# Performance work log

Hardware: AMD Instinct MI355X
Metric: run time of the kernel (lower is better)

Reference implementation:

```python
import jax, jax.numpy as jnp
import numpy as np

B = 32768
C = 1000


def setup_inputs() -> dict:
    key = jax.random.key(0)
    k1, k2, k3 = jax.random.split(key, 3)
    output = jax.random.normal(k1, (B, C), dtype=jnp.float32)
    target = jax.random.randint(k2, (B,), 0, C, dtype=jnp.int64)
    # loss_lams rows are (approx) probability vectors from the previous epoch
    lams = jax.random.uniform(k3, (C, C), dtype=jnp.float32)
    loss_lams = lams / jnp.sum(lams, axis=1, keepdims=True)
    return {"output": output, "target": target, "loss_lams": loss_lams}


def reference(output, target, loss_lams):
    """OLS loss forward.

    Returns (loss, cur_epoch_lams_update, cur_epoch_cnt_update) where the
    updates are the increments added to the zero-initialized per-epoch state
    (update_loss_lams side effect), and loss = 0.5*CE + 0.5*softCE.
    """
    b, c = output.shape
    target = target.astype(jnp.int32)

    # --- update_loss_lams: softmax, keep samples where argmax == target,
    # scatter-add their prob vectors into the row of their target class ---
    probs = jax.nn.softmax(output, axis=1)                      # [B, C]
    pred = jnp.argmax(probs, axis=1)                            # [B]
    correct = (pred == target).astype(output.dtype)             # [B]
    lams_update = jax.ops.segment_sum(probs * correct[:, None], target,
                                      num_segments=c)           # [C, C]
    cnt_update = jax.ops.segment_sum(correct, target, num_segments=c)  # [C]

    # --- loss: 0.5 * hard CE + 0.5 * soft CE with loss_lams soft labels ---
    log_probs = jax.nn.log_softmax(output, axis=1)              # [B, C]
    ce = -jnp.mean(jnp.take_along_axis(log_probs, target[:, None], axis=1))
    soft_targets = loss_lams[target]                            # [B, C] gather
    soft_ce = -jnp.sum(log_probs * soft_targets) / b
    loss = 0.5 * ce + 0.5 * soft_ce
    return loss, lams_update, cnt_update
```

## Files before the change

### kernel.cpp

```cpp
#include <hip/hip_runtime.h>
#include <math.h>

constexpr int B_ROWS = 32768;
constexpr int C_COLS = 1000;
constexpr int VEC4   = C_COLS / 4;

using f4 = __attribute__((ext_vector_type(4))) float;

__global__ __launch_bounds__(256, 8) void ols_main(
    const float* __restrict__ output,
    const int*   __restrict__ target,
    const float* __restrict__ lams,
    float*       __restrict__ partials,
    float*       __restrict__ lams_upd,
    float*       __restrict__ cnt_upd)
{
    __shared__ float s_max[4];
    __shared__ float s_red[4][3];
    __shared__ float s_xt;

    const int tid  = threadIdx.x;
    const int lane = tid & 63;
    const int wid  = tid >> 6;
    const int row  = blockIdx.x;
    const bool act = tid < VEC4;

    const int t = target[row];

    f4 x = act ? reinterpret_cast<const f4*>(output + (size_t)row * C_COLS)[tid]
               : (f4){-INFINITY, -INFINITY, -INFINITY, -INFINITY};
    f4 l = act ? reinterpret_cast<const f4*>(lams + (size_t)t * C_COLS)[tid]
               : (f4){0.0f, 0.0f, 0.0f, 0.0f};

    float m = fmaxf(fmaxf(x[0], x[1]), fmaxf(x[2], x[3]));
#pragma unroll
    for (int off = 32; off > 0; off >>= 1) m = fmaxf(m, __shfl_xor(m, off));
    if (lane == 0) s_max[wid] = m;

    const int q = t >> 2, e = t & 3;
    if (tid == q)
        s_xt = (e == 0) ? x[0] : (e == 1) ? x[1] : (e == 2) ? x[2] : x[3];
    __syncthreads();

    m = fmaxf(fmaxf(s_max[0], s_max[1]), fmaxf(s_max[2], s_max[3]));
    const float x_t = s_xt;

    float p0 = __expf(x[0] - m), p1 = __expf(x[1] - m);
    float p2 = __expf(x[2] - m), p3 = __expf(x[3] - m);
    float s   = (p0 + p1) + (p2 + p3);
    float dot = act ? (l[0]*x[0] + l[1]*x[1]) + (l[2]*x[2] + l[3]*x[3]) : 0.0f;
    float rs  = (l[0] + l[1]) + (l[2] + l[3]);
#pragma unroll
    for (int off = 32; off > 0; off >>= 1) {
        s   += __shfl_xor(s,   off);
        dot += __shfl_xor(dot, off);
        rs  += __shfl_xor(rs,  off);
    }
    if (lane == 0) { s_red[wid][0] = s; s_red[wid][1] = dot; s_red[wid][2] = rs; }
    __syncthreads();

    s = (s_red[0][0] + s_red[1][0]) + (s_red[2][0] + s_red[3][0]);

    if (tid == 0) {
        const float dT = (s_red[0][1] + s_red[1][1]) + (s_red[2][1] + s_red[3][1]);
        const float rT = (s_red[0][2] + s_red[1][2]) + (s_red[2][2] + s_red[3][2]);
        const float lse = m + __logf(s);
        partials[row] = 0.5f * ((lse - x_t) + (lse * rT - dT));
    }

    if (x_t == m) {
        const float inv = 1.0f / s;
        if (act) {
            float* dst = lams_upd + (size_t)t * C_COLS + 4 * tid;
            atomicAdd(dst + 0, p0 * inv);
            atomicAdd(dst + 1, p1 * inv);
            atomicAdd(dst + 2, p2 * inv);
            atomicAdd(dst + 3, p3 * inv);
        }
        if (tid == 0) atomicAdd(&cnt_upd[t], 1.0f);
    }
}

__global__ __launch_bounds__(256) void ols_reduce(
    const float* __restrict__ partials, float* __restrict__ d_loss)
{
    __shared__ float sm[4];
    const int lane = threadIdx.x & 63;
    const int wid  = threadIdx.x >> 6;
    const f4* p4 = reinterpret_cast<const f4*>(partials);
    float acc = 0.0f;
#pragma unroll
    for (int k = 0; k < 32; ++k) {
        f4 v = p4[threadIdx.x + k * 256];
        acc += (v[0] + v[1]) + (v[2] + v[3]);
    }
#pragma unroll
    for (int off = 32; off > 0; off >>= 1) acc += __shfl_xor(acc, off);
    if (lane == 0) sm[wid] = acc;
    __syncthreads();
    if (threadIdx.x == 0)
        *d_loss = ((sm[0] + sm[1]) + (sm[2] + sm[3])) * (1.0f / (float)B_ROWS);
}

extern "C" void kernel_launch(void* const* d_in, const int* in_sizes, int n_in,
                              void* d_out, int out_size, void* d_ws, size_t ws_size,
                              hipStream_t stream) {
    const float* output = (const float*)d_in[0];
    const int*   target = (const int*)d_in[1];
    const float* lams   = (const float*)d_in[2];

    float* out      = (float*)d_out;
    float* d_loss   = out;
    float* lams_upd = out + 1;
    float* cnt_upd  = out + 1 + C_COLS * C_COLS;
    float* partials = (float*)d_ws;

    hipMemsetAsync(d_out, 0, (size_t)out_size * sizeof(float), stream);

    ols_main<<<dim3(B_ROWS), dim3(256), 0, stream>>>(output, target, lams,
                                                     partials, lams_upd, cnt_upd);
    ols_reduce<<<dim3(1), dim3(256), 0, stream>>>(partials, d_loss);
}
```

Before: 202.2 us.

## Process multiple rows per block with register prefetch and single-barrier online softmax

Launches 2048 persistent-style blocks that each loop over 16 rows, prefetching the next row's logits and target into registers while the current row is processed. The block max is no longer a separate barrier step: each wave keeps its own max, and the per-wave sums are rescaled, which cuts the row's two syncthreads to one. Loss is accumulated per block, so the final reduce reads 2048 partials instead of 32768. The cost is a less parallel grid and extra exp calls, and the lams gather still waits on the target load with no prefetch.

After: 205.6 us. No clear change (+1.7%).

```diff
diff --git a/kernel.cpp b/kernel.cpp
--- a/kernel.cpp
+++ b/kernel.cpp
@@ -4,6 +4,8 @@
 constexpr int B_ROWS = 32768;
 constexpr int C_COLS = 1000;
 constexpr int VEC4   = C_COLS / 4;
+constexpr int NBLK   = 2048;
+constexpr int RPB    = B_ROWS / NBLK;
 
 using f4 = __attribute__((ext_vector_type(4))) float;
 
@@ -15,70 +17,98 @@
     float*       __restrict__ lams_upd,
     float*       __restrict__ cnt_upd)
 {
-    __shared__ float s_max[4];
-    __shared__ float s_red[4][3];
-    __shared__ float s_xt;
+    __shared__ float s_stat[2][4][4];
+    __shared__ float s_xt[2];
 
     const int tid  = threadIdx.x;
     const int lane = tid & 63;
     const int wid  = tid >> 6;
-    const int row  = blockIdx.x;
     const bool act = tid < VEC4;
 
-    const int t = target[row];
+    const f4 X_PAD = (f4){-INFINITY, -INFINITY, -INFINITY, -INFINITY};
 
-    f4 x = act ? reinterpret_cast<const f4*>(output + (size_t)row * C_COLS)[tid]
-               : (f4){-INFINITY, -INFINITY, -INFINITY, -INFINITY};
-    f4 l = act ? reinterpret_cast<const f4*>(lams + (size_t)t * C_COLS)[tid]
-               : (f4){0.0f, 0.0f, 0.0f, 0.0f};
+    float lossAcc = 0.0f;
 
-    float m = fmaxf(fmaxf(x[0], x[1]), fmaxf(x[2], x[3]));
+    int tb[2];
+    f4  xb[2];
+    tb[0] = target[blockIdx.x];
+    xb[0] = act ? reinterpret_cast<const f4*>(output + (size_t)blockIdx.x * C_COLS)[tid]
+                : X_PAD;
+
 #pragma unroll
-    for (int off = 32; off > 0; off >>= 1) m = fmaxf(m, __shfl_xor(m, off));
-    if (lane == 0) s_max[wid] = m;
+    for (int i = 0; i < RPB; ++i) {
+        const int cb = i & 1, nb = cb ^ 1;
 
-    const int q = t >> 2, e = t & 3;
-    if (tid == q)
-        s_xt = (e == 0) ? x[0] : (e == 1) ? x[1] : (e == 2) ? x[2] : x[3];
-    __syncthreads();
+        if (i + 1 < RPB) {
+            const int nrow = blockIdx.x + (i + 1) * NBLK;
+            tb[nb] = target[nrow];
+            xb[nb] = act ? reinterpret_cast<const f4*>(output + (size_t)nrow * C_COLS)[tid]
+                         : X_PAD;
+        }
 
-    m = fmaxf(fmaxf(s_max[0], s_max[1]), fmaxf(s_max[2], s_max[3]));
-    const float x_t = s_xt;
+        const int t = tb[cb];
+        const f4  x = xb[cb];
 
-    float p0 = __expf(x[0] - m), p1 = __expf(x[1] - m);
-    float p2 = __expf(x[2] - m), p3 = __expf(x[3] - m);
-    float s   = (p0 + p1) + (p2 + p3);
-    float dot = act ? (l[0]*x[0] + l[1]*x[1]) + (l[2]*x[2] + l[3]*x[3]) : 0.0f;
-    float rs  = (l[0] + l[1]) + (l[2] + l[3]);
+        const f4 l = act ? reinterpret_cast<const f4*>(lams + (size_t)t * C_COLS)[tid]
+                         : (f4){0.0f, 0.0f, 0.0f, 0.0f};
+
+        float mw = fmaxf(fmaxf(x[0], x[1]), fmaxf(x[2], x[3]));
 #pragma unroll
-    for (int off = 32; off > 0; off >>= 1) {
-        s   += __shfl_xor(s,   off);
-        dot += __shfl_xor(dot, off);
-        rs  += __shfl_xor(rs,  off);
-    }
-    if (lane == 0) { s_red[wid][0] = s; s_red[wid][1] = dot; s_red[wid][2] = rs; }
-    __syncthreads();
+        for (int off = 32; off > 0; off >>= 1) mw = fmaxf(mw, __shfl_xor(mw, off));
 
-    s = (s_red[0][0] + s_red[1][0]) + (s_red[2][0] + s_red[3][0]);
+        const float p0 = __expf(x[0] - mw), p1 = __expf(x[1] - mw);
+        const float p2 = __expf(x[2] - mw), p3 = __expf(x[3] - mw);
+        float s = (p0 + p1) + (p2 + p3);
+        float dot = act ? (l[0]*x[0] + l[1]*x[1]) + (l[2]*x[2] + l[3]*x[3]) : 0.0f;
+        float rs  = (l[0] + l[1]) + (l[2] + l[3]);
+#pragma unroll
+        for (int off = 32; off > 0; off >>= 1) {
+            s   += __shfl_xor(s,   off);
+            dot += __shfl_xor(dot, off);
+            rs  += __shfl_xor(rs,  off);
+        }
+        if (lane == 0) {
+            s_stat[cb][wid][0] = mw; s_stat[cb][wid][1] = s;
+            s_stat[cb][wid][2] = dot; s_stat[cb][wid][3] = rs;
+        }
+        if (tid == (t >> 2)) {
+            const int e = t & 3;
+            s_xt[cb] = (e == 0) ? x[0] : (e == 1) ? x[1] : (e == 2) ? x[2] : x[3];
+        }
+        __syncthreads();
 
-    if (tid == 0) {
-        const float dT = (s_red[0][1] + s_red[1][1]) + (s_red[2][1] + s_red[3][1]);
-        const float rT = (s_red[0][2] + s_red[1][2]) + (s_red[2][2] + s_red[3][2]);
-        const float lse = m + __logf(s);
-        partials[row] = 0.5f * ((lse - x_t) + (lse * rT - dT));
+        const float m0 = s_stat[cb][0][0], m1 = s_stat[cb][1][0];
+        const float m2 = s_stat[cb][2][0], m3 = s_stat[cb][3][0];
+        const float m  = fmaxf(fmaxf(m0, m1), fmaxf(m2, m3));
+        const float S  = s_stat[cb][0][1] * __expf(m0 - m)
+                       + s_stat[cb][1][1] * __expf(m1 - m)
+                       + s_stat[cb][2][1] * __expf(m2 - m)
+                       + s_stat[cb][3][1] * __expf(m3 - m);
+        const float x_t = s_xt[cb];
+
+        if (tid == 0) {
+            const float D = (s_stat[cb][0][2] + s_stat[cb][1][2])
+                          + (s_stat[cb][2][2] + s_stat[cb][3][2]);
+            const float R = (s_stat[cb][0][3] + s_stat[cb][1][3])
+                          + (s_stat[cb][2][3] + s_stat[cb][3][3]);
+            const float lse = m + __logf(S);
+            lossAcc += 0.5f * ((lse - x_t) + (lse * R - D));
+        }
+
+        if (x_t == m) {
+            const float scale = __expf(s_stat[cb][wid][0] - m) / S;
+            if (act) {
+                float* dst = lams_upd + (size_t)t * C_COLS + 4 * tid;
+                atomicAdd(dst + 0, p0 * scale);
+                atomicAdd(dst + 1, p1 * scale);
+                atomicAdd(dst + 2, p2 * scale);
+                atomicAdd(dst + 3, p3 * scale);
+            }
+            if (tid == 0) atomicAdd(&cnt_upd[t], 1.0f);
+        }
     }
 
-    if (x_t == m) {
-        const float inv = 1.0f / s;
-        if (act) {
-            float* dst = lams_upd + (size_t)t * C_COLS + 4 * tid;
-            atomicAdd(dst + 0, p0 * inv);
-            atomicAdd(dst + 1, p1 * inv);
-            atomicAdd(dst + 2, p2 * inv);
-            atomicAdd(dst + 3, p3 * inv);
-        }
-        if (tid == 0) atomicAdd(&cnt_upd[t], 1.0f);
-    }
+    if (tid == 0) partials[blockIdx.x] = lossAcc;
 }
 
 __global__ __launch_bounds__(256) void ols_reduce(
@@ -88,12 +118,9 @@
     const int lane = threadIdx.x & 63;
     const int wid  = threadIdx.x >> 6;
     const f4* p4 = reinterpret_cast<const f4*>(partials);
-    float acc = 0.0f;
-#pragma unroll
-    for (int k = 0; k < 32; ++k) {
-        f4 v = p4[threadIdx.x + k * 256];
-        acc += (v[0] + v[1]) + (v[2] + v[3]);
-    }
+    f4 a = p4[threadIdx.x];
+    f4 b = p4[threadIdx.x + 256];
+    float acc = ((a[0] + a[1]) + (a[2] + a[3])) + ((b[0] + b[1]) + (b[2] + b[3]));
 #pragma unroll
     for (int off = 32; off > 0; off >>= 1) acc += __shfl_xor(acc, off);
     if (lane == 0) sm[wid] = acc;
@@ -117,7 +144,7 @@
 
     hipMemsetAsync(d_out, 0, (size_t)out_size * sizeof(float), stream);
 
-    ols_main<<<dim3(B_ROWS), dim3(256), 0, stream>>>(output, target, lams,
-                                                     partials, lams_upd, cnt_upd);
+    ols_main<<<dim3(NBLK), dim3(256), 0, stream>>>(output, target, lams,
+                                                   partials, lams_upd, cnt_upd);
     ols_reduce<<<dim3(1), dim3(256), 0, stream>>>(partials, d_loss);
 }
```
